# Kernel optimization log

Measured on AMD Instinct MI355X. Metric: run time of the kernel, lower is better.

The kernel has to match this reference:

```python
import jax, jax.numpy as jnp
import numpy as np

HID = 32

def _lstm_step(x, h, c, W_ih, W_hh):
    # PyTorch LSTMCell, no bias. gates: [i, f, g, o] chunks of size HID
    gates = x @ W_ih.T + h @ W_hh.T  # (B, 4*HID)
    i, f, g, o = jnp.split(gates, 4, axis=1)
    i = jax.nn.sigmoid(i)
    f = jax.nn.sigmoid(f)
    g = jnp.tanh(g)
    o = jax.nn.sigmoid(o)
    c_new = f * c + i * g
    h_new = o * jnp.tanh(c_new)
    return h_new, c_new

def setup_inputs() -> dict:
    key = jax.random.key(0)
    ks = jax.random.split(key, 5)
    T, B = 64, 65536
    poses = jax.random.normal(ks[0], (T, B, 4), dtype=jnp.float32)
    deltas = jax.random.uniform(ks[1], (T, B), dtype=jnp.float32)
    W_ih = jax.random.normal(ks[2], (4 * HID, 4), dtype=jnp.float32) * (1.0 / np.sqrt(HID))
    W_hh = jax.random.normal(ks[3], (4 * HID, HID), dtype=jnp.float32) * (1.0 / np.sqrt(HID))
    W_dense = jax.random.normal(ks[4], (3, HID), dtype=jnp.float32) * (1.0 / np.sqrt(HID))
    return {"poses": poses, "deltas": deltas, "W_ih": W_ih, "W_hh": W_hh,
            "W_dense": W_dense, "n_new_poses": T}

def reference(poses, deltas, W_ih, W_hh, W_dense, n_new_poses):
    B = poses.shape[1]
    # zip(poses, deltas) truncates encode loop to min length (source semantics)
    T_enc = min(poses.shape[0], deltas.shape[0])
    h0 = jnp.zeros((B, HID), dtype=poses.dtype)
    c0 = jnp.zeros((B, HID), dtype=poses.dtype)

    def enc_step(carry, pose):
        h, c = carry
        h, c = _lstm_step(pose, h, c, W_ih, W_hh)
        return (h, c), None

    (h, c), _ = jax.lax.scan(enc_step, (h0, c0), poses[:T_enc])

    last_velocity = h @ W_dense.T  # (B, 3)
    last_pose = poses[-1]          # (B, 4)

    def dec_step(carry, dt):
        h, c, pose, vel = carry
        cs, sn = vel[:, 1], vel[:, 2]
        norm = jnp.sqrt(cs * cs + sn * sn)
        cs = cs / norm
        sn = sn / norm
        # NOTE: source uses non-in-place .add -> positions are NOT updated; dt unused
        new_pose = jnp.concatenate([pose[:, :2], cs[:, None], sn[:, None]], axis=1)
        h, c = _lstm_step(new_pose, h, c, W_ih, W_hh)
        vel = h @ W_dense.T
        return (h, c, new_pose, vel), new_pose

    _, pred_poses = jax.lax.scan(dec_step, (h, c, last_pose, last_velocity),
                                 deltas[:n_new_poses])
    return pred_poses  # (n_new_poses, B, 4)
```

## Files before the change

kernel.cpp:

```cpp
#include <hip/hip_runtime.h>

typedef float v2f __attribute__((ext_vector_type(2)));

#define HID 32
#define LOG2E 1.4426950408889634f

#if __has_builtin(__builtin_amdgcn_exp2f)
#define EXP2(x) __builtin_amdgcn_exp2f(x)
#else
#define EXP2(x) exp2f(x)
#endif
#if __has_builtin(__builtin_amdgcn_rcpf)
#define RCP(x) __builtin_amdgcn_rcpf(x)
#else
#define RCP(x) (1.0f / (x))
#endif

#define PKFMA(acc, w, h) \
    asm("v_pk_fma_f32 %0, %1, %2, %0" : "+v"(acc) : "v"(w), "v"(h))

#define SWZ_ADD(p, imm) do {                                            \
    int _t = __builtin_amdgcn_ds_swizzle(__float_as_int(p), (imm));     \
    (p) += __int_as_float(_t); } while (0)
#define REDUCE32(p) do {                                                \
    SWZ_ADD(p, 0x041F); SWZ_ADD(p, 0x081F); SWZ_ADD(p, 0x101F);        \
    SWZ_ADD(p, 0x201F); SWZ_ADD(p, 0x401F); } while (0)

__global__ __attribute__((amdgpu_waves_per_eu(3, 4))) __launch_bounds__(256)
void lstm_gatesplit(const float* __restrict__ poses,
                    const float* __restrict__ W_ih,
                    const float* __restrict__ W_hh,
                    const float* __restrict__ W_dense,
                    float* __restrict__ out,
                    int B, int T_enc, int T_dec)
{
    __shared__ __align__(16) float hx[4][HID];

    const int tid  = threadIdx.x;
    const int lane = tid & 63;
    const int wv   = tid >> 6;
    const int k    = lane & 31;
    const int isH  = lane >> 5;
    const int el   = blockIdx.x * 4 + wv;

    const int rowA = isH * 32 + k;
    const int rowB = rowA + 64;

    const v2f* Wih2 = reinterpret_cast<const v2f*>(W_ih);
    v2f wA0 = Wih2[2 * rowA], wA1 = Wih2[2 * rowA + 1];
    v2f wB0 = Wih2[2 * rowB], wB1 = Wih2[2 * rowB + 1];
    v2f whhA[16], whhB[16];
    {
        const v2f* Whh2 = reinterpret_cast<const v2f*>(W_hh);
        #pragma unroll
        for (int j = 0; j < 16; ++j) {
            whhA[j] = Whh2[rowA * 16 + j];
            whhB[j] = Whh2[rowB * 16 + j];
        }
    }
    const float wd1 = W_dense[HID + k];
    const float wd2 = W_dense[2 * HID + k];

    const float S1 = isH ? -LOG2E : 2.0f * LOG2E;
    const float A1 = isH ? 0.0f : 1.0f;
    const float B1 = isH ? 1.0f : -2.0f;

    v2f h2[16];
    #pragma unroll
    for (int j = 0; j < 16; ++j) h2[j] = (v2f){0.f, 0.f};
    float c = 0.f, hk = 0.f;

    const float4* poses4 = reinterpret_cast<const float4*>(poses);
    float4*       out4   = reinterpret_cast<float4*>(out);

    auto lstm_step = [&](v2f x01, v2f x23) {
        v2f aA = {0.f, 0.f}, aB = {0.f, 0.f};
        PKFMA(aA, wA0, x01); PKFMA(aA, wA1, x23);
        PKFMA(aB, wB0, x01); PKFMA(aB, wB1, x23);
        #pragma unroll
        for (int j = 0; j < 16; ++j) {
            PKFMA(aA, whhA[j], h2[j]);
            PKFMA(aB, whhB[j], h2[j]);
        }
        const float a0 = aA.x + aA.y;
        const float a1 = aB.x + aB.y;
        const float act0 = RCP(1.0f + EXP2(-LOG2E * a0));
        const float act1 = fmaf(B1, RCP(1.0f + EXP2(S1 * a1)), A1);
        const float xo0 = __shfl_xor(act0, 32, 64);
        const float xo1 = __shfl_xor(act1, 32, 64);
        const float i_ = isH ? xo0  : act0;
        const float f_ = isH ? act0 : xo0;
        const float g_ = isH ? xo1  : act1;
        const float o_ = isH ? act1 : xo1;
        c = fmaf(f_, c, i_ * g_);
        const float th = fmaf(-2.0f, RCP(1.0f + EXP2((2.0f * LOG2E) * c)), 1.0f);
        hk = o_ * th;
        if (!isH) hx[wv][k] = hk;
        const v2f* hr = reinterpret_cast<const v2f*>(&hx[wv][0]);
        #pragma unroll
        for (int j = 0; j < 16; ++j) h2[j] = hr[j];
    };

    float4 x = poses4[el];
    for (int t = 0; t < T_enc; ++t) {
        float4 xn = x;
        if (t + 1 < T_enc) xn = poses4[(size_t)(t + 1) * B + el];
        lstm_step((v2f){x.x, x.y}, (v2f){x.z, x.w});
        x = xn;
    }
    const v2f p01 = {x.x, x.y};

    float v1 = wd1 * hk, v2 = wd2 * hk;
    REDUCE32(v1); REDUCE32(v2);

    for (int t = 0; t < T_dec; ++t) {
        const float rn = rsqrtf(v1 * v1 + v2 * v2);
        const float cs = v1 * rn, sn = v2 * rn;
        if (lane == 0) out4[(size_t)t * B + el] = make_float4(p01.x, p01.y, cs, sn);
        lstm_step(p01, (v2f){cs, sn});
        v1 = wd1 * hk; v2 = wd2 * hk;
        REDUCE32(v1); REDUCE32(v2);
    }
}

extern "C" void kernel_launch(void* const* d_in, const int* in_sizes, int n_in,
                              void* d_out, int out_size, void* d_ws, size_t ws_size,
                              hipStream_t stream) {
    const float* poses   = (const float*)d_in[0];
    const float* W_ih    = (const float*)d_in[2];
    const float* W_hh    = (const float*)d_in[3];
    const float* W_dense = (const float*)d_in[4];
    float* out = (float*)d_out;

    const int T_enc = 64;
    const int B     = in_sizes[0] / (T_enc * 4);
    const int T_dec = out_size / (B * 4);

    dim3 grid(B / 4), block(256);
    hipLaunchKernelGGL(lstm_gatesplit, grid, block, 0, stream,
                       poses, W_ih, W_hh, W_dense, out, B, T_enc, T_dec);
}
```

Baseline: 1.506 ms.

## Process two batch elements per wavefront to reuse register-resident weights

```diff
diff --git a/kernel.cpp b/kernel.cpp
--- a/kernel.cpp
+++ b/kernel.cpp
@@ -16,8 +16,7 @@
 #define RCP(x) (1.0f / (x))
 #endif
 
-#define PKFMA(acc, w, h) \
-    asm("v_pk_fma_f32 %0, %1, %2, %0" : "+v"(acc) : "v"(w), "v"(h))
+#define PKFMA(acc, w, h) (acc) = __builtin_elementwise_fma((w), (h), (acc))
 
 #define SWZ_ADD(p, imm) do {                                            \
     int _t = __builtin_amdgcn_ds_swizzle(__float_as_int(p), (imm));     \
@@ -26,22 +25,23 @@
     SWZ_ADD(p, 0x041F); SWZ_ADD(p, 0x081F); SWZ_ADD(p, 0x101F);        \
     SWZ_ADD(p, 0x201F); SWZ_ADD(p, 0x401F); } while (0)
 
-__global__ __attribute__((amdgpu_waves_per_eu(3, 4))) __launch_bounds__(256)
-void lstm_gatesplit(const float* __restrict__ poses,
-                    const float* __restrict__ W_ih,
-                    const float* __restrict__ W_hh,
-                    const float* __restrict__ W_dense,
-                    float* __restrict__ out,
-                    int B, int T_enc, int T_dec)
+__global__ __attribute__((amdgpu_waves_per_eu(2, 2))) __launch_bounds__(256)
+void lstm_dual(const float* __restrict__ poses,
+               const float* __restrict__ W_ih,
+               const float* __restrict__ W_hh,
+               const float* __restrict__ W_dense,
+               float* __restrict__ out,
+               int B, int T_enc, int T_dec)
 {
-    __shared__ __align__(16) float hx[4][HID];
+    __shared__ __align__(16) float hx[4][2][HID];
 
     const int tid  = threadIdx.x;
     const int lane = tid & 63;
     const int wv   = tid >> 6;
     const int k    = lane & 31;
     const int isH  = lane >> 5;
-    const int el   = blockIdx.x * 4 + wv;
+    const int el0  = (blockIdx.x * 4 + wv) * 2;
+    const int el1  = el0 + 1;
 
     const int rowA = isH * 32 + k;
     const int rowB = rowA + 64;
@@ -65,23 +65,17 @@
     const float A1 = isH ? 0.0f : 1.0f;
     const float B1 = isH ? 1.0f : -2.0f;
 
-    v2f h2[16];
+    v2f h2a[16], h2b[16];
     #pragma unroll
-    for (int j = 0; j < 16; ++j) h2[j] = (v2f){0.f, 0.f};
-    float c = 0.f, hk = 0.f;
+    for (int j = 0; j < 16; ++j) { h2a[j] = (v2f){0.f, 0.f}; h2b[j] = (v2f){0.f, 0.f}; }
+    float c0 = 0.f, c1 = 0.f, hk0 = 0.f, hk1 = 0.f;
 
     const float4* poses4 = reinterpret_cast<const float4*>(poses);
     float4*       out4   = reinterpret_cast<float4*>(out);
 
-    auto lstm_step = [&](v2f x01, v2f x23) {
-        v2f aA = {0.f, 0.f}, aB = {0.f, 0.f};
-        PKFMA(aA, wA0, x01); PKFMA(aA, wA1, x23);
-        PKFMA(aB, wB0, x01); PKFMA(aB, wB1, x23);
-        #pragma unroll
-        for (int j = 0; j < 16; ++j) {
-            PKFMA(aA, whhA[j], h2[j]);
-            PKFMA(aB, whhB[j], h2[j]);
-        }
+    float* __restrict__ hrow = &hx[wv][0][0];
+
+    auto finish = [&](v2f aA, v2f aB, float& c, float& hk) {
         const float a0 = aA.x + aA.y;
         const float a1 = aB.x + aB.y;
         const float act0 = RCP(1.0f + EXP2(-LOG2E * a0));
@@ -95,31 +89,66 @@
         c = fmaf(f_, c, i_ * g_);
         const float th = fmaf(-2.0f, RCP(1.0f + EXP2((2.0f * LOG2E) * c)), 1.0f);
         hk = o_ * th;
-        if (!isH) hx[wv][k] = hk;
-        const v2f* hr = reinterpret_cast<const v2f*>(&hx[wv][0]);
-        #pragma unroll
-        for (int j = 0; j < 16; ++j) h2[j] = hr[j];
     };
 
-    float4 x = poses4[el];
+    auto step = [&](v2f aA0, v2f aB0, v2f aA1, v2f aB1) {
+        #pragma unroll
+        for (int j = 0; j < 16; ++j) {
+            PKFMA(aA0, whhA[j], h2a[j]);
+            PKFMA(aB0, whhB[j], h2a[j]);
+            PKFMA(aA1, whhA[j], h2b[j]);
+            PKFMA(aB1, whhB[j], h2b[j]);
+        }
+        finish(aA0, aB0, c0, hk0);
+        finish(aA1, aB1, c1, hk1);
+        hrow[lane] = isH ? hk1 : hk0;
+        const v2f* hr = reinterpret_cast<const v2f*>(hrow);
+        #pragma unroll
+        for (int j = 0; j < 16; ++j) { h2a[j] = hr[j]; h2b[j] = hr[16 + j]; }
+    };
+
+    const float4* pp = poses4 + el0;
+    float4 x0 = pp[0], x1 = pp[1];
     for (int t = 0; t < T_enc; ++t) {
-        float4 xn = x;
-        if (t + 1 < T_enc) xn = poses4[(size_t)(t + 1) * B + el];
-        lstm_step((v2f){x.x, x.y}, (v2f){x.z, x.w});
-        x = xn;
+        pp += B;
+        float4 xn0 = x0, xn1 = x1;
+        if (t + 1 < T_enc) { xn0 = pp[0]; xn1 = pp[1]; }
+        v2f aA0 = {0.f, 0.f}, aB0 = {0.f, 0.f}, aA1 = {0.f, 0.f}, aB1 = {0.f, 0.f};
+        const v2f x001 = {x0.x, x0.y}, x023 = {x0.z, x0.w};
+        const v2f x101 = {x1.x, x1.y}, x123 = {x1.z, x1.w};
+        PKFMA(aA0, wA0, x001); PKFMA(aA0, wA1, x023);
+        PKFMA(aB0, wB0, x001); PKFMA(aB0, wB1, x023);
+        PKFMA(aA1, wA0, x101); PKFMA(aA1, wA1, x123);
+        PKFMA(aB1, wB0, x101); PKFMA(aB1, wB1, x123);
+        step(aA0, aB0, aA1, aB1);
+        x0 = xn0; x1 = xn1;
     }
-    const v2f p01 = {x.x, x.y};
+    const v2f p001 = {x0.x, x0.y};
+    const v2f p101 = {x1.x, x1.y};
 
-    float v1 = wd1 * hk, v2 = wd2 * hk;
-    REDUCE32(v1); REDUCE32(v2);
+    float v10 = wd1 * hk0, v20 = wd2 * hk0;
+    float v11 = wd1 * hk1, v21 = wd2 * hk1;
+    REDUCE32(v10); REDUCE32(v20); REDUCE32(v11); REDUCE32(v21);
+
+    v2f bA0 = {0.f, 0.f}, bB0 = {0.f, 0.f}, bA1 = {0.f, 0.f}, bB1 = {0.f, 0.f};
+    PKFMA(bA0, wA0, p001); PKFMA(bB0, wB0, p001);
+    PKFMA(bA1, wA0, p101); PKFMA(bB1, wB0, p101);
 
     for (int t = 0; t < T_dec; ++t) {
-        const float rn = rsqrtf(v1 * v1 + v2 * v2);
-        const float cs = v1 * rn, sn = v2 * rn;
-        if (lane == 0) out4[(size_t)t * B + el] = make_float4(p01.x, p01.y, cs, sn);
-        lstm_step(p01, (v2f){cs, sn});
-        v1 = wd1 * hk; v2 = wd2 * hk;
-        REDUCE32(v1); REDUCE32(v2);
+        const float rn0 = rsqrtf(v10 * v10 + v20 * v20);
+        const float cs0 = v10 * rn0, sn0 = v20 * rn0;
+        const float rn1 = rsqrtf(v11 * v11 + v21 * v21);
+        const float cs1 = v11 * rn1, sn1 = v21 * rn1;
+        if (lane == 0) out4[(size_t)t * B + el0] = make_float4(p001.x, p001.y, cs0, sn0);
+        if (lane == 1) out4[(size_t)t * B + el1] = make_float4(p101.x, p101.y, cs1, sn1);
+        v2f aA0 = bA0, aB0 = bB0, aA1 = bA1, aB1 = bB1;
+        const v2f cssn0 = {cs0, sn0}, cssn1 = {cs1, sn1};
+        PKFMA(aA0, wA1, cssn0); PKFMA(aB0, wB1, cssn0);
+        PKFMA(aA1, wA1, cssn1); PKFMA(aB1, wB1, cssn1);
+        step(aA0, aB0, aA1, aB1);
+        v10 = wd1 * hk0; v20 = wd2 * hk0;
+        v11 = wd1 * hk1; v21 = wd2 * hk1;
+        REDUCE32(v10); REDUCE32(v20); REDUCE32(v11); REDUCE32(v21);
     }
 }
 
@@ -136,7 +165,7 @@
     const int B     = in_sizes[0] / (T_enc * 4);
     const int T_dec = out_size / (B * 4);
 
-    dim3 grid(B / 4), block(256);
-    hipLaunchKernelGGL(lstm_gatesplit, grid, block, 0, stream,
+    dim3 grid(B / 8), block(256);
+    hipLaunchKernelGGL(lstm_dual, grid, block, 0, stream,
                        poses, W_ih, W_hh, W_dense, out, B, T_enc, T_dec);
 }
```

Measured after the change: 1.436 ms. -4.7%, faster.
